# Performance work log

Measured on AMD Instinct MI355X. Metric: run time of the kernel, lower is better.

The kernel has to match this reference:

```python
import jax, jax.numpy as jnp
import numpy as np

B, N, L, E = 4096, 64, 256, 256


def setup_inputs() -> dict:
    key = jax.random.key(0)
    k1, k2, k3, k4, k5, k6 = jax.random.split(key, 6)
    return {
        "agent_latent": jax.random.normal(k1, (B, L), dtype=jnp.float32),
        "opponent_latents": jax.random.normal(k2, (B, N, L), dtype=jnp.float32),
        "hard_attention": jax.random.uniform(k3, (B, N), dtype=jnp.float32),
        "Ws": jax.random.normal(k4, (E, L), dtype=jnp.float32) * (2.0 / (L + E)) ** 0.5,
        "Wt": jax.random.normal(k5, (E, L), dtype=jnp.float32) * (2.0 / (L + E)) ** 0.5,
        "Wc": jax.random.normal(k6, (E, L), dtype=jnp.float32) * (2.0 / (L + E)) ** 0.5,
    }


def reference(agent_latent, opponent_latents, hard_attention, Ws, Wt, Wc):
    # agent embedding: [B, E]  (nn.Linear: x @ W.T)
    a = agent_latent @ Ws.T
    # opponent key embedding: [B, N, E]
    emb_t = jnp.einsum('bnl,el->bne', opponent_latents, Wt)
    # bmm([B,N,E],[B,E,1]) -> [B,N]
    scores = jnp.einsum('bne,be->bn', emb_t, a)
    scores = jax.nn.softmax(scores, axis=-1) * hard_attention
    # opponent value embedding: [B, N, E]
    emb_c = jnp.einsum('bnl,el->bne', opponent_latents, Wc)
    # broadcast-multiply + sum over opponents -> [B, E]
    result = jnp.einsum('bn,bne->be', scores, emb_c)
    return result, scores
```

## Files before the change

kernel.cpp:

```cpp
#include <hip/hip_runtime.h>


#define Bsz 4096
#define Nn  64
#define Ll  256
#define Ee  256

__global__ __launch_bounds__(256) void prep_kernel(
    const float* __restrict__ Ws, const float* __restrict__ Wt,
    const float* __restrict__ Wc, float* __restrict__ MT, float* __restrict__ WcT) {
  int col = threadIdx.x;
  int row = blockIdx.x;
  if (row < 256) {
    float acc = 0.f;
    for (int e = 0; e < 256; ++e)
      acc = fmaf(Ws[e * 256 + row], Wt[e * 256 + col], acc);
    MT[row * 256 + col] = acc;
  } else {
    int l = row - 256;
    WcT[l * 256 + col] = Wc[col * 256 + l];
  }
}

__global__ __launch_bounds__(256) void rowmat_kernel(
    const float* __restrict__ in, const float* __restrict__ W, float* __restrict__ out) {
  __shared__ float v_s[16 * 256];
  const int tid = threadIdx.x;
  const int b0 = blockIdx.x * 16;
  const int j  = blockIdx.y * 64 + (tid & 63);
  const int g  = (tid >> 6) * 4;

  const float4* in4 = (const float4*)(in + (size_t)b0 * 256);
  float4* s4 = (float4*)v_s;
#pragma unroll
  for (int i = 0; i < 4; ++i) s4[i * 256 + tid] = in4[i * 256 + tid];
  __syncthreads();

  float acc[4] = {0.f, 0.f, 0.f, 0.f};
  for (int k4 = 0; k4 < 64; ++k4) {
    const float w0 = W[(k4 * 4 + 0) * 256 + j];
    const float w1 = W[(k4 * 4 + 1) * 256 + j];
    const float w2 = W[(k4 * 4 + 2) * 256 + j];
    const float w3 = W[(k4 * 4 + 3) * 256 + j];
#pragma unroll
    for (int i = 0; i < 4; ++i) {
      const float4 vv = ((const float4*)(v_s + (g + i) * 256))[k4];
      acc[i] = fmaf(vv.x, w0, fmaf(vv.y, w1, fmaf(vv.z, w2, fmaf(vv.w, w3, acc[i]))));
    }
  }
#pragma unroll
  for (int i = 0; i < 4; ++i) out[(size_t)(b0 + g + i) * 256 + j] = acc[i];
}

__global__ __launch_bounds__(256, 2) void fused_kernel(
    const float* __restrict__ opp, const float* __restrict__ T,
    const float* __restrict__ hard, float* __restrict__ scores_out,
    float* __restrict__ V) {
  __shared__ float opp_s[Nn * Ll];
  __shared__ float t_s[Ll];
  __shared__ float sraw[Nn];
  __shared__ float sfin[Nn];

  const int b = blockIdx.x;
  const int tid = threadIdx.x;
  const int lane = tid & 63;
  const int wave = tid >> 6;

  const float4* o4 = (const float4*)(opp + (size_t)b * (Nn * Ll));
  float4* os4 = (float4*)opp_s;
#pragma unroll
  for (int i = 0; i < 16; ++i) os4[i * 256 + tid] = o4[i * 256 + tid];
  t_s[tid] = T[(size_t)b * Ll + tid];
  __syncthreads();

  const float4 tv = ((const float4*)t_s)[lane];
  for (int jj = 0; jj < 16; ++jj) {
    const int n = wave * 16 + jj;
    const float4 ov = ((const float4*)(opp_s + n * Ll))[lane];
    float p = ov.x * tv.x + ov.y * tv.y + ov.z * tv.z + ov.w * tv.w;
#pragma unroll
    for (int off = 32; off; off >>= 1) p += __shfl_down(p, off, 64);
    if (lane == 0) sraw[n] = p;
  }
  __syncthreads();

  if (tid < 64) {
    const float x = sraw[tid];
    float m = x;
#pragma unroll
    for (int off = 32; off; off >>= 1) m = fmaxf(m, __shfl_xor(m, off, 64));
    const float e = __expf(x - m);
    float s = e;
#pragma unroll
    for (int off = 32; off; off >>= 1) s += __shfl_xor(s, off, 64);
    const float val = e / s * hard[(size_t)b * Nn + tid];
    sfin[tid] = val;
    scores_out[(size_t)b * Nn + tid] = val;
  }
  __syncthreads();

  float acc = 0.f;
#pragma unroll
  for (int n = 0; n < Nn; ++n) acc = fmaf(sfin[n], opp_s[n * Ll + tid], acc);
  V[(size_t)b * Ll + tid] = acc;
}

extern "C" void kernel_launch(void* const* d_in, const int* in_sizes, int n_in,
                              void* d_out, int out_size, void* d_ws, size_t ws_size,
                              hipStream_t stream) {
  const float* agent = (const float*)d_in[0];
  const float* opp   = (const float*)d_in[1];
  const float* hard  = (const float*)d_in[2];
  const float* Ws    = (const float*)d_in[3];
  const float* Wt    = (const float*)d_in[4];
  const float* Wc    = (const float*)d_in[5];

  float* out = (float*)d_out;
  float* scores_out = out + (size_t)Bsz * Ee;

  float* ws  = (float*)d_ws;
  float* MT  = ws;
  float* WcT = MT + 65536;
  float* T   = WcT + 65536;
  float* V   = T + (size_t)Bsz * Ll;

  prep_kernel<<<512, 256, 0, stream>>>(Ws, Wt, Wc, MT, WcT);
  rowmat_kernel<<<dim3(Bsz / 16, 4), 256, 0, stream>>>(agent, MT, T);
  fused_kernel<<<Bsz, 256, 0, stream>>>(opp, T, hard, scores_out, V);
  rowmat_kernel<<<dim3(Bsz / 16, 4), 256, 0, stream>>>(V, WcT, out);
}
```

Measured before the change: 456.0 us.

## Load opponent tile directly to LDS and vectorize weighted-sum reduction

Replaces the register-staged copy of the 64x256 opponent tile into shared memory with direct global-to-LDS loads, so the data skips VGPRs and can be issued with fewer instructions. The final weighted sum over opponents is restructured so each wave handles 16 opponents with float4 LDS reads, then partial sums are combined through shared memory. This cuts LDS read instructions but adds an extra barrier and reduction step. The direct LDS load depends on the builtin's lane-to-address mapping being correct for 16-byte transfers.

```diff
diff --git a/kernel.cpp b/kernel.cpp
--- a/kernel.cpp
+++ b/kernel.cpp
@@ -5,6 +5,13 @@
 #define Nn  64
 #define Ll  256
 #define Ee  256
+
+__device__ __forceinline__ void gload_lds16(const float4* g, float4* lds_base) {
+  __builtin_amdgcn_global_load_lds(
+      (const __attribute__((address_space(1))) unsigned int*)g,
+      (__attribute__((address_space(3))) unsigned int*)lds_base,
+      16, 0, 0);
+}
 
 __global__ __launch_bounds__(256) void prep_kernel(
     const float* __restrict__ Ws, const float* __restrict__ Wt,
@@ -69,7 +76,8 @@
   const float4* o4 = (const float4*)(opp + (size_t)b * (Nn * Ll));
   float4* os4 = (float4*)opp_s;
 #pragma unroll
-  for (int i = 0; i < 16; ++i) os4[i * 256 + tid] = o4[i * 256 + tid];
+  for (int i = 0; i < 16; ++i)
+    gload_lds16(o4 + i * 256 + wave * 64 + lane, os4 + i * 256 + wave * 64);
   t_s[tid] = T[(size_t)b * Ll + tid];
   __syncthreads();
 
@@ -99,10 +107,34 @@
   }
   __syncthreads();
 
-  float acc = 0.f;
+  const int q = wave;
+  const int l0 = (tid & 63) * 4;
+  float4 acc = {0.f, 0.f, 0.f, 0.f};
 #pragma unroll
-  for (int n = 0; n < Nn; ++n) acc = fmaf(sfin[n], opp_s[n * Ll + tid], acc);
-  V[(size_t)b * Ll + tid] = acc;
+  for (int k = 0; k < 16; ++k) {
+    const int n = q * 16 + k;
+    const float s = sfin[n];
+    const float4 ov = *(const float4*)(opp_s + n * Ll + l0);
+    acc.x = fmaf(s, ov.x, acc.x);
+    acc.y = fmaf(s, ov.y, acc.y);
+    acc.z = fmaf(s, ov.z, acc.z);
+    acc.w = fmaf(s, ov.w, acc.w);
+  }
+  __syncthreads();
+  float4* part = (float4*)opp_s;
+  part[q * 64 + (tid & 63)] = acc;
+  __syncthreads();
+  if (tid < 64) {
+    float4 r = part[tid];
+    const float4 r1 = part[64 + tid];
+    const float4 r2 = part[128 + tid];
+    const float4 r3 = part[192 + tid];
+    r.x += r1.x + r2.x + r3.x;
+    r.y += r1.y + r2.y + r3.y;
+    r.z += r1.z + r2.z + r3.z;
+    r.w += r1.w + r2.w + r3.w;
+    ((float4*)(V + (size_t)b * Ll))[tid] = r;
+  }
 }
 
 extern "C" void kernel_launch(void* const* d_in, const int* in_sizes, int n_in,
```

Result: no change. 454.2 us (-0.4%).

## Use direct global-to-LDS loads and retile rowmat for float4 weight reuse

Applied to the files above, without the earlier changes.

The opponent tile in the fused kernel is now loaded with direct global-to-LDS 16-byte transfers, and the agent projection is read straight from global memory instead of staged through LDS. The row-matrix kernel is retiled so each thread computes a 2-row by 4-column block with vectorised weight loads, and each block covers all 256 columns for 8 rows. This is meant to cut register staging of the large opponent tile and raise the FMA-to-load ratio in the small GEMMs. It depends on the hardware supporting 16-byte global_load_lds and on proper wait handling before the barrier.

```diff
diff --git a/kernel.cpp b/kernel.cpp
--- a/kernel.cpp
+++ b/kernel.cpp
@@ -5,6 +5,13 @@
 #define Nn  64
 #define Ll  256
 #define Ee  256
+
+__device__ __forceinline__ void gload_lds16(const float4* g, float4* lds_base) {
+  __builtin_amdgcn_global_load_lds(
+      (const __attribute__((address_space(1))) unsigned int*)g,
+      (__attribute__((address_space(3))) unsigned int*)lds_base,
+      16, 0, 0);
+}
 
 __global__ __launch_bounds__(256) void prep_kernel(
     const float* __restrict__ Ws, const float* __restrict__ Wt,
@@ -24,32 +31,38 @@
 
 __global__ __launch_bounds__(256) void rowmat_kernel(
     const float* __restrict__ in, const float* __restrict__ W, float* __restrict__ out) {
-  __shared__ float v_s[16 * 256];
+  __shared__ float in_s[8 * 256];
   const int tid = threadIdx.x;
-  const int b0 = blockIdx.x * 16;
-  const int j  = blockIdx.y * 64 + (tid & 63);
-  const int g  = (tid >> 6) * 4;
+  const int b0 = blockIdx.x * 8;
+  const int jq = tid & 63;
+  const int r0 = (tid >> 6) * 2;
 
   const float4* in4 = (const float4*)(in + (size_t)b0 * 256);
-  float4* s4 = (float4*)v_s;
+  float4* s4 = (float4*)in_s;
 #pragma unroll
-  for (int i = 0; i < 4; ++i) s4[i * 256 + tid] = in4[i * 256 + tid];
+  for (int i = 0; i < 2; ++i) s4[i * 256 + tid] = in4[i * 256 + tid];
   __syncthreads();
 
-  float acc[4] = {0.f, 0.f, 0.f, 0.f};
+  float4 acc0 = {0.f, 0.f, 0.f, 0.f};
+  float4 acc1 = {0.f, 0.f, 0.f, 0.f};
   for (int k4 = 0; k4 < 64; ++k4) {
-    const float w0 = W[(k4 * 4 + 0) * 256 + j];
-    const float w1 = W[(k4 * 4 + 1) * 256 + j];
-    const float w2 = W[(k4 * 4 + 2) * 256 + j];
-    const float w3 = W[(k4 * 4 + 3) * 256 + j];
-#pragma unroll
-    for (int i = 0; i < 4; ++i) {
-      const float4 vv = ((const float4*)(v_s + (g + i) * 256))[k4];
-      acc[i] = fmaf(vv.x, w0, fmaf(vv.y, w1, fmaf(vv.z, w2, fmaf(vv.w, w3, acc[i]))));
-    }
+    const float4 w0 = ((const float4*)(W + (k4 * 4 + 0) * 256))[jq];
+    const float4 w1 = ((const float4*)(W + (k4 * 4 + 1) * 256))[jq];
+    const float4 w2 = ((const float4*)(W + (k4 * 4 + 2) * 256))[jq];
+    const float4 w3 = ((const float4*)(W + (k4 * 4 + 3) * 256))[jq];
+    const float4 v0 = ((const float4*)(in_s + (r0 + 0) * 256))[k4];
+    const float4 v1 = ((const float4*)(in_s + (r0 + 1) * 256))[k4];
+    acc0.x = fmaf(v0.x, w0.x, fmaf(v0.y, w1.x, fmaf(v0.z, w2.x, fmaf(v0.w, w3.x, acc0.x))));
+    acc0.y = fmaf(v0.x, w0.y, fmaf(v0.y, w1.y, fmaf(v0.z, w2.y, fmaf(v0.w, w3.y, acc0.y))));
+    acc0.z = fmaf(v0.x, w0.z, fmaf(v0.y, w1.z, fmaf(v0.z, w2.z, fmaf(v0.w, w3.z, acc0.z))));
+    acc0.w = fmaf(v0.x, w0.w, fmaf(v0.y, w1.w, fmaf(v0.z, w2.w, fmaf(v0.w, w3.w, acc0.w))));
+    acc1.x = fmaf(v1.x, w0.x, fmaf(v1.y, w1.x, fmaf(v1.z, w2.x, fmaf(v1.w, w3.x, acc1.x))));
+    acc1.y = fmaf(v1.x, w0.y, fmaf(v1.y, w1.y, fmaf(v1.z, w2.y, fmaf(v1.w, w3.y, acc1.y))));
+    acc1.z = fmaf(v1.x, w0.z, fmaf(v1.y, w1.z, fmaf(v1.z, w2.z, fmaf(v1.w, w3.z, acc1.z))));
+    acc1.w = fmaf(v1.x, w0.w, fmaf(v1.y, w1.w, fmaf(v1.z, w2.w, fmaf(v1.w, w3.w, acc1.w))));
   }
-#pragma unroll
-  for (int i = 0; i < 4; ++i) out[(size_t)(b0 + g + i) * 256 + j] = acc[i];
+  ((float4*)(out + (size_t)(b0 + r0 + 0) * 256))[jq] = acc0;
+  ((float4*)(out + (size_t)(b0 + r0 + 1) * 256))[jq] = acc1;
 }
 
 __global__ __launch_bounds__(256, 2) void fused_kernel(
@@ -57,7 +70,6 @@
     const float* __restrict__ hard, float* __restrict__ scores_out,
     float* __restrict__ V) {
   __shared__ float opp_s[Nn * Ll];
-  __shared__ float t_s[Ll];
   __shared__ float sraw[Nn];
   __shared__ float sfin[Nn];
 
@@ -69,11 +81,12 @@
   const float4* o4 = (const float4*)(opp + (size_t)b * (Nn * Ll));
   float4* os4 = (float4*)opp_s;
 #pragma unroll
-  for (int i = 0; i < 16; ++i) os4[i * 256 + tid] = o4[i * 256 + tid];
-  t_s[tid] = T[(size_t)b * Ll + tid];
+  for (int i = 0; i < 16; ++i)
+    gload_lds16(o4 + i * 256 + wave * 64 + lane, os4 + i * 256 + wave * 64);
+
+  const float4 tv = ((const float4*)(T + (size_t)b * Ll))[lane];
   __syncthreads();
 
-  const float4 tv = ((const float4*)t_s)[lane];
   for (int jj = 0; jj < 16; ++jj) {
     const int n = wave * 16 + jj;
     const float4 ov = ((const float4*)(opp_s + n * Ll))[lane];
@@ -125,7 +138,7 @@
   float* V   = T + (size_t)Bsz * Ll;
 
   prep_kernel<<<512, 256, 0, stream>>>(Ws, Wt, Wc, MT, WcT);
-  rowmat_kernel<<<dim3(Bsz / 16, 4), 256, 0, stream>>>(agent, MT, T);
+  rowmat_kernel<<<dim3(Bsz / 8, 1), 256, 0, stream>>>(agent, MT, T);
   fused_kernel<<<Bsz, 256, 0, stream>>>(opp, T, hard, scores_out, V);
-  rowmat_kernel<<<dim3(Bsz / 16, 4), 256, 0, stream>>>(V, WcT, out);
+  rowmat_kernel<<<dim3(Bsz / 8, 1), 256, 0, stream>>>(V, WcT, out);
 }
```

Result: faster. 442.8 us (-2.9%).

## Fuse agent projection, attention, and value projection into one mega kernel

Applied to the files above, without the earlier changes.

Replaces the three kernels (agent@MT rowmat, per-batch attention, V@WcT rowmat) with a single kernel in which each block processes 8 batch rows. The T and V intermediates stay in shared memory instead of round-tripping through global memory, and the opponent tiles are loaded with global_load_lds direct-to-LDS copies. The cost is that the grid shrinks to 512 blocks and each block works through its 8 rows serially with many barriers and no overlap between loading and computing. The rowmat phases also reuse each MT/WcT weight load across only 2 rows per wave, so weight traffic may rise.

```diff
diff --git a/kernel.cpp b/kernel.cpp
--- a/kernel.cpp
+++ b/kernel.cpp
@@ -5,6 +5,13 @@
 #define Nn  64
 #define Ll  256
 #define Ee  256
+
+__device__ __forceinline__ void gload_lds16(const float4* g, float4* lds_base) {
+  __builtin_amdgcn_global_load_lds(
+      (const __attribute__((address_space(1))) unsigned int*)g,
+      (__attribute__((address_space(3))) unsigned int*)lds_base,
+      16, 0, 0);
+}
 
 __global__ __launch_bounds__(256) void prep_kernel(
     const float* __restrict__ Ws, const float* __restrict__ Wt,
@@ -22,87 +29,126 @@
   }
 }
 
-__global__ __launch_bounds__(256) void rowmat_kernel(
-    const float* __restrict__ in, const float* __restrict__ W, float* __restrict__ out) {
-  __shared__ float v_s[16 * 256];
-  const int tid = threadIdx.x;
-  const int b0 = blockIdx.x * 16;
-  const int j  = blockIdx.y * 64 + (tid & 63);
-  const int g  = (tid >> 6) * 4;
-
-  const float4* in4 = (const float4*)(in + (size_t)b0 * 256);
-  float4* s4 = (float4*)v_s;
-#pragma unroll
-  for (int i = 0; i < 4; ++i) s4[i * 256 + tid] = in4[i * 256 + tid];
-  __syncthreads();
-
-  float acc[4] = {0.f, 0.f, 0.f, 0.f};
-  for (int k4 = 0; k4 < 64; ++k4) {
-    const float w0 = W[(k4 * 4 + 0) * 256 + j];
-    const float w1 = W[(k4 * 4 + 1) * 256 + j];
-    const float w2 = W[(k4 * 4 + 2) * 256 + j];
-    const float w3 = W[(k4 * 4 + 3) * 256 + j];
-#pragma unroll
-    for (int i = 0; i < 4; ++i) {
-      const float4 vv = ((const float4*)(v_s + (g + i) * 256))[k4];
-      acc[i] = fmaf(vv.x, w0, fmaf(vv.y, w1, fmaf(vv.z, w2, fmaf(vv.w, w3, acc[i]))));
-    }
-  }
-#pragma unroll
-  for (int i = 0; i < 4; ++i) out[(size_t)(b0 + g + i) * 256 + j] = acc[i];
-}
-
-__global__ __launch_bounds__(256, 2) void fused_kernel(
-    const float* __restrict__ opp, const float* __restrict__ T,
-    const float* __restrict__ hard, float* __restrict__ scores_out,
-    float* __restrict__ V) {
+__global__ __launch_bounds__(256, 2) void mega_kernel(
+    const float* __restrict__ agent, const float* __restrict__ opp,
+    const float* __restrict__ hard, const float* __restrict__ MT,
+    const float* __restrict__ WcT, float* __restrict__ out,
+    float* __restrict__ scores_out) {
   __shared__ float opp_s[Nn * Ll];
-  __shared__ float t_s[Ll];
+  __shared__ float V_s[8 * Ll];
   __shared__ float sraw[Nn];
   __shared__ float sfin[Nn];
 
-  const int b = blockIdx.x;
   const int tid = threadIdx.x;
   const int lane = tid & 63;
   const int wave = tid >> 6;
+  const int b0 = blockIdx.x * 8;
 
-  const float4* o4 = (const float4*)(opp + (size_t)b * (Nn * Ll));
+  const int jq = lane;
+  const int r0 = wave * 2;
+
+  float* ag_s  = opp_s;
+  float* T_tmp = opp_s + 2048;
+  {
+    const float4* in4 = (const float4*)(agent + (size_t)b0 * 256);
+    float4* s4 = (float4*)ag_s;
+    s4[tid] = in4[tid];
+    s4[256 + tid] = in4[256 + tid];
+    __syncthreads();
+
+    float4 a0 = {0.f, 0.f, 0.f, 0.f};
+    float4 a1 = {0.f, 0.f, 0.f, 0.f};
+    for (int k4 = 0; k4 < 64; ++k4) {
+      const float4 w0 = ((const float4*)(MT + (k4 * 4 + 0) * 256))[jq];
+      const float4 w1 = ((const float4*)(MT + (k4 * 4 + 1) * 256))[jq];
+      const float4 w2 = ((const float4*)(MT + (k4 * 4 + 2) * 256))[jq];
+      const float4 w3 = ((const float4*)(MT + (k4 * 4 + 3) * 256))[jq];
+      const float4 v0 = ((const float4*)(ag_s + (r0 + 0) * 256))[k4];
+      const float4 v1 = ((const float4*)(ag_s + (r0 + 1) * 256))[k4];
+      a0.x = fmaf(v0.x, w0.x, fmaf(v0.y, w1.x, fmaf(v0.z, w2.x, fmaf(v0.w, w3.x, a0.x))));
+      a0.y = fmaf(v0.x, w0.y, fmaf(v0.y, w1.y, fmaf(v0.z, w2.y, fmaf(v0.w, w3.y, a0.y))));
+      a0.z = fmaf(v0.x, w0.z, fmaf(v0.y, w1.z, fmaf(v0.z, w2.z, fmaf(v0.w, w3.z, a0.z))));
+      a0.w = fmaf(v0.x, w0.w, fmaf(v0.y, w1.w, fmaf(v0.z, w2.w, fmaf(v0.w, w3.w, a0.w))));
+      a1.x = fmaf(v1.x, w0.x, fmaf(v1.y, w1.x, fmaf(v1.z, w2.x, fmaf(v1.w, w3.x, a1.x))));
+      a1.y = fmaf(v1.x, w0.y, fmaf(v1.y, w1.y, fmaf(v1.z, w2.y, fmaf(v1.w, w3.y, a1.y))));
+      a1.z = fmaf(v1.x, w0.z, fmaf(v1.y, w1.z, fmaf(v1.z, w2.z, fmaf(v1.w, w3.z, a1.z))));
+      a1.w = fmaf(v1.x, w0.w, fmaf(v1.y, w1.w, fmaf(v1.z, w2.w, fmaf(v1.w, w3.w, a1.w))));
+    }
+    __syncthreads();
+    ((float4*)(T_tmp + (r0 + 0) * 256))[jq] = a0;
+    ((float4*)(T_tmp + (r0 + 1) * 256))[jq] = a1;
+    __syncthreads();
+  }
+  float4 tv[8];
+#pragma unroll
+  for (int i = 0; i < 8; ++i) tv[i] = ((const float4*)(T_tmp + i * 256))[lane];
+  __syncthreads();
+
+  const float4* o4base = (const float4*)(opp + (size_t)b0 * (Nn * Ll));
   float4* os4 = (float4*)opp_s;
 #pragma unroll
-  for (int i = 0; i < 16; ++i) os4[i * 256 + tid] = o4[i * 256 + tid];
-  t_s[tid] = T[(size_t)b * Ll + tid];
-  __syncthreads();
+  for (int i = 0; i < 8; ++i) {
+    const float4* o4 = o4base + (size_t)i * 4096;
+#pragma unroll
+    for (int k = 0; k < 16; ++k)
+      gload_lds16(o4 + k * 256 + wave * 64 + lane, os4 + k * 256 + wave * 64);
+    __syncthreads();
 
-  const float4 tv = ((const float4*)t_s)[lane];
-  for (int jj = 0; jj < 16; ++jj) {
-    const int n = wave * 16 + jj;
-    const float4 ov = ((const float4*)(opp_s + n * Ll))[lane];
-    float p = ov.x * tv.x + ov.y * tv.y + ov.z * tv.z + ov.w * tv.w;
+    const float4 tvi = tv[i];
+    for (int jj = 0; jj < 16; ++jj) {
+      const int n = wave * 16 + jj;
+      const float4 ov = ((const float4*)(opp_s + n * Ll))[lane];
+      float p = ov.x * tvi.x + ov.y * tvi.y + ov.z * tvi.z + ov.w * tvi.w;
 #pragma unroll
-    for (int off = 32; off; off >>= 1) p += __shfl_down(p, off, 64);
-    if (lane == 0) sraw[n] = p;
+      for (int off = 32; off; off >>= 1) p += __shfl_down(p, off, 64);
+      if (lane == 0) sraw[n] = p;
+    }
+    __syncthreads();
+
+    if (tid < 64) {
+      const float x = sraw[tid];
+      float m = x;
+#pragma unroll
+      for (int off = 32; off; off >>= 1) m = fmaxf(m, __shfl_xor(m, off, 64));
+      const float e = __expf(x - m);
+      float s = e;
+#pragma unroll
+      for (int off = 32; off; off >>= 1) s += __shfl_xor(s, off, 64);
+      const float val = e / s * hard[(size_t)(b0 + i) * Nn + tid];
+      sfin[tid] = val;
+      scores_out[(size_t)(b0 + i) * Nn + tid] = val;
+    }
+    __syncthreads();
+
+    float acc = 0.f;
+#pragma unroll
+    for (int n = 0; n < Nn; ++n) acc = fmaf(sfin[n], opp_s[n * Ll + tid], acc);
+    V_s[i * Ll + tid] = acc;
+    __syncthreads();
   }
-  __syncthreads();
 
-  if (tid < 64) {
-    const float x = sraw[tid];
-    float m = x;
-#pragma unroll
-    for (int off = 32; off; off >>= 1) m = fmaxf(m, __shfl_xor(m, off, 64));
-    const float e = __expf(x - m);
-    float s = e;
-#pragma unroll
-    for (int off = 32; off; off >>= 1) s += __shfl_xor(s, off, 64);
-    const float val = e / s * hard[(size_t)b * Nn + tid];
-    sfin[tid] = val;
-    scores_out[(size_t)b * Nn + tid] = val;
+  {
+    float4 a0 = {0.f, 0.f, 0.f, 0.f};
+    float4 a1 = {0.f, 0.f, 0.f, 0.f};
+    for (int k4 = 0; k4 < 64; ++k4) {
+      const float4 w0 = ((const float4*)(WcT + (k4 * 4 + 0) * 256))[jq];
+      const float4 w1 = ((const float4*)(WcT + (k4 * 4 + 1) * 256))[jq];
+      const float4 w2 = ((const float4*)(WcT + (k4 * 4 + 2) * 256))[jq];
+      const float4 w3 = ((const float4*)(WcT + (k4 * 4 + 3) * 256))[jq];
+      const float4 v0 = ((const float4*)(V_s + (r0 + 0) * 256))[k4];
+      const float4 v1 = ((const float4*)(V_s + (r0 + 1) * 256))[k4];
+      a0.x = fmaf(v0.x, w0.x, fmaf(v0.y, w1.x, fmaf(v0.z, w2.x, fmaf(v0.w, w3.x, a0.x))));
+      a0.y = fmaf(v0.x, w0.y, fmaf(v0.y, w1.y, fmaf(v0.z, w2.y, fmaf(v0.w, w3.y, a0.y))));
+      a0.z = fmaf(v0.x, w0.z, fmaf(v0.y, w1.z, fmaf(v0.z, w2.z, fmaf(v0.w, w3.z, a0.z))));
+      a0.w = fmaf(v0.x, w0.w, fmaf(v0.y, w1.w, fmaf(v0.z, w2.w, fmaf(v0.w, w3.w, a0.w))));
+      a1.x = fmaf(v1.x, w0.x, fmaf(v1.y, w1.x, fmaf(v1.z, w2.x, fmaf(v1.w, w3.x, a1.x))));
+      a1.y = fmaf(v1.x, w0.y, fmaf(v1.y, w1.y, fmaf(v1.z, w2.y, fmaf(v1.w, w3.y, a1.y))));
+      a1.z = fmaf(v1.x, w0.z, fmaf(v1.y, w1.z, fmaf(v1.z, w2.z, fmaf(v1.w, w3.z, a1.z))));
+      a1.w = fmaf(v1.x, w0.w, fmaf(v1.y, w1.w, fmaf(v1.z, w2.w, fmaf(v1.w, w3.w, a1.w))));
+    }
+    ((float4*)(out + (size_t)(b0 + r0 + 0) * 256))[jq] = a0;
+    ((float4*)(out + (size_t)(b0 + r0 + 1) * 256))[jq] = a1;
   }
-  __syncthreads();
-
-  float acc = 0.f;
-#pragma unroll
-  for (int n = 0; n < Nn; ++n) acc = fmaf(sfin[n], opp_s[n * Ll + tid], acc);
-  V[(size_t)b * Ll + tid] = acc;
 }
 
 extern "C" void kernel_launch(void* const* d_in, const int* in_sizes, int n_in,
@@ -121,11 +167,7 @@
   float* ws  = (float*)d_ws;
   float* MT  = ws;
   float* WcT = MT + 65536;
-  float* T   = WcT + 65536;
-  float* V   = T + (size_t)Bsz * Ll;
 
   prep_kernel<<<512, 256, 0, stream>>>(Ws, Wt, Wc, MT, WcT);
-  rowmat_kernel<<<dim3(Bsz / 16, 4), 256, 0, stream>>>(agent, MT, T);
-  fused_kernel<<<Bsz, 256, 0, stream>>>(opp, T, hard, scores_out, V);
-  rowmat_kernel<<<dim3(Bsz / 16, 4), 256, 0, stream>>>(V, WcT, out);
+  mega_kernel<<<Bsz / 8, 256, 0, stream>>>(agent, opp, hard, MT, WcT, out, scores_out);
 }
```

Result: faster. 420.2 us (-7.9%).
